# Optimization experiments

Hardware: AMD Instinct MI355X
Metric: run time of the kernel (lower is better)

Reference implementation:

```python
import jax, jax.numpy as jnp
import numpy as np

B, N, M, C1, C2 = 8, 8192, 2048, 64, 128
MLP = [128, 128]
EPS = 1e-5


def setup_inputs() -> dict:
    key = jax.random.key(0)
    ks = jax.random.split(key, 12)
    inp = {
        'low_theta': jax.random.normal(ks[0], (B, N), jnp.float32),
        'low_phi': jax.random.normal(ks[1], (B, N), jnp.float32),
        'low_feats': jax.random.normal(ks[2], (B, C1, N), jnp.float32),
        'high_theta': jax.random.normal(ks[3], (B, M), jnp.float32),
        'high_phi': jax.random.normal(ks[4], (B, M), jnp.float32),
        'high_feats': jax.random.normal(ks[5], (B, C2, M), jnp.float32),
    }
    in_ch = C1 + C2
    # layer 0: conv1d (kernel size 1) -> weight [out, in], bias [out]; BN gamma/beta
    inp['W0'] = jax.random.normal(ks[6], (MLP[0], in_ch), jnp.float32) * 0.05
    inp['b0'] = jnp.zeros((MLP[0],), jnp.float32)
    inp['g0'] = jnp.ones((MLP[0],), jnp.float32)
    inp['beta0'] = jnp.zeros((MLP[0],), jnp.float32)
    # layer 1
    inp['W1'] = jax.random.normal(ks[7], (MLP[1], MLP[0]), jnp.float32) * 0.05
    inp['b1'] = jnp.zeros((MLP[1],), jnp.float32)
    inp['g1'] = jnp.ones((MLP[1],), jnp.float32)
    inp['beta1'] = jnp.zeros((MLP[1],), jnp.float32)
    return inp


def _conv_bn_relu(x, W, b, gamma, beta):
    # x: [B, Cin, N] -> 1x1 conv -> BN (training-mode batch stats, biased var) -> ReLU
    y = jnp.einsum('oi,bin->bon', W, x) + b[None, :, None]
    mean = jnp.mean(y, axis=(0, 2), keepdims=True)
    var = jnp.mean((y - mean) ** 2, axis=(0, 2), keepdims=True)
    yhat = (y - mean) * jax.lax.rsqrt(var + EPS)
    return jax.nn.relu(gamma[None, :, None] * yhat + beta[None, :, None])


def reference(low_theta, low_phi, low_feats, high_theta, high_phi, high_feats,
              W0, b0, g0, beta0, W1, b1, g1, beta1):
    # pairwise angular distance [B, N, M]
    dtheta = low_theta[:, :, None] - high_theta[:, None, :]
    dphi = low_phi[:, :, None] - high_phi[:, None, :]
    dist = jnp.sqrt(dtheta ** 2 + dphi ** 2)
    idx = jnp.argmin(dist, axis=-1)  # [B, N]
    # gather nearest-neighbor high features -> [B, C2, N]
    c2 = high_feats.shape[1]
    interpolated = jnp.take_along_axis(
        high_feats, jnp.broadcast_to(idx[:, None, :], (idx.shape[0], c2, idx.shape[1])), axis=2)
    cat = jnp.concatenate([low_feats, interpolated], axis=1)  # [B, C1+C2, N]
    h = _conv_bn_relu(cat, W0, b0, g0, beta0)
    out = _conv_bn_relu(h, W1, b1, g1, beta1)
    return out
```

## Files before the change

### kernel.cpp

```cpp
#include <hip/hip_runtime.h>
#include <hip/hip_bf16.h>

#define BB 8
#define NN 8192
#define MM 2048
#define C1 64
#define C2 128
#define CIN 192
#define CO 128
#define NB (BB*NN)
#define EPS 1e-5f

typedef unsigned short u16;
typedef unsigned int u32;
typedef __bf16 bf16_t;
typedef bf16_t bf16x8 __attribute__((ext_vector_type(8)));
typedef float f32x4 __attribute__((ext_vector_type(4)));

static __device__ __forceinline__ float b2f(u16 u) { return __uint_as_float(((u32)u) << 16); }
static __device__ __forceinline__ u16 f2b(float f) {
    __hip_bfloat16 h = __float2bfloat16(f);
    u16 u; __builtin_memcpy(&u, &h, 2); return u;
}

__global__ void k_prep_w(const float* __restrict__ W0, const float* __restrict__ W1,
                         u16* __restrict__ W0b, u16* __restrict__ W1b) {
    int t = blockIdx.x * 256 + threadIdx.x;
    if (t < CIN * CO) W0b[t] = f2b(W0[t]);
    if (t < CO * CO)  W1b[t] = f2b(W1[t]);
}

__global__ void k_prep_h(const float* __restrict__ hf, u16* __restrict__ hT) {
    __shared__ u16 s[64][65];
    int b = blockIdx.x, m0 = blockIdx.y * 64, c0 = blockIdx.z * 64;
    for (int e = threadIdx.x; e < 64 * 64; e += 256) {
        int i = e >> 6, j = e & 63;
        s[i][j] = f2b(hf[(b * C2 + c0 + i) * MM + m0 + j]);
    }
    __syncthreads();
    for (int e = threadIdx.x; e < 64 * 64; e += 256) {
        int ii = e & 63, jj = e >> 6;
        hT[(b * MM + m0 + jj) * C2 + c0 + ii] = s[ii][jj];
    }
}

__global__ __launch_bounds__(256) void k_argmin(
        const float* __restrict__ lt_, const float* __restrict__ lp_,
        const float* __restrict__ ht_, const float* __restrict__ hp_,
        int* __restrict__ idx) {
    __shared__ float2 hs[8 * 260];
    int b = blockIdx.x >> 8;
    int n0 = (blockIdx.x & 255) << 5;
    int tid = threadIdx.x;
    for (int e = tid; e < MM; e += 256) {
        int p = e >> 8, i = e & 255;
        hs[p * 260 + i] = make_float2(ht_[b * MM + e], hp_[b * MM + e]);
    }
    __syncthreads();
    int q = tid >> 3, p = tid & 7;
    float lt = lt_[b * NN + n0 + q];
    float lp = lp_[b * NN + n0 + q];
    float dl[4] = {1e30f, 1e30f, 1e30f, 1e30f};
    float dpv[4] = {1e30f, 1e30f, 1e30f, 1e30f};
    int il[4] = {0, 0, 0, 0}, ip[4] = {0, 0, 0, 0};
    const float2* hp2 = &hs[p * 260];
    int mbase = p << 8;
#pragma unroll 8
    for (int i4 = 0; i4 < 64; ++i4) {
#pragma unroll
        for (int c = 0; c < 4; ++c) {
            float2 h = hp2[i4 * 4 + c];
            float dt = lt - h.x, dp = lp - h.y;
            float d2 = __fadd_rn(__fmul_rn(dt, dt), __fmul_rn(dp, dp));
            bool hit = d2 < dl[c];
            dpv[c] = hit ? dl[c] : dpv[c];
            ip[c] = hit ? il[c] : ip[c];
            dl[c] = hit ? d2 : dl[c];
            il[c] = hit ? mbase + i4 * 4 + c : il[c];
        }
    }
    float bs = 1e30f; int bm = 0x7fffffff;
#pragma unroll
    for (int c = 0; c < 4; ++c) {
        float sl = __fsqrt_rn(dl[c]);
        float sp = __fsqrt_rn(dpv[c]);
        int cand = (sp == sl) ? ip[c] : il[c];
        if (sl < bs || (sl == bs && cand < bm)) { bs = sl; bm = cand; }
    }
#pragma unroll
    for (int d = 1; d <= 4; d <<= 1) {
        float ov = __shfl_xor(bs, d, 64);
        int om = __shfl_xor(bm, d, 64);
        if (ov < bs || (ov == bs && om < bm)) { bs = ov; bm = om; }
    }
    if (p == 0) idx[b * NN + n0 + q] = bm;
}

static __device__ __forceinline__ void epilogue(
        f32x4* ac0, f32x4* ac1, const float* bias, u16* yl,
        float* chs, float* chq, int w, int ln, int q) {
#pragma unroll
    for (int mf = 0; mf < 2; ++mf) {
        f32x4* A = mf ? ac1 : ac0;
        int chb = 32 * w + 16 * mf + 4 * q;
        float bs[4], ss[4] = {0.f, 0.f, 0.f, 0.f}, sq[4] = {0.f, 0.f, 0.f, 0.f};
#pragma unroll
        for (int r = 0; r < 4; ++r) bs[r] = bias[chb + r];
#pragma unroll
        for (int nf = 0; nf < 4; ++nf) {
            int n = (nf << 4) + ln;
#pragma unroll
            for (int r = 0; r < 4; ++r) {
                float y = A[nf][r] + bs[r];
                ss[r] += y; sq[r] += y * y;
                int o = chb + r;
                yl[(o << 6) + (n ^ ((o & 7) << 3))] = f2b(y);
            }
        }
#pragma unroll
        for (int r = 0; r < 4; ++r) {
            float v = ss[r], u2 = sq[r];
#pragma unroll
            for (int d = 1; d < 16; d <<= 1) {
                v += __shfl_xor(v, d, 64);
                u2 += __shfl_xor(u2, d, 64);
            }
            if (ln == 0) { atomicAdd(&chs[chb + r], v); atomicAdd(&chq[chb + r], u2); }
        }
    }
}

__global__ __launch_bounds__(256) void k_red(const float* __restrict__ gpart,
                                             float* __restrict__ gout) {
    __shared__ float part[4];
    int c = blockIdx.x;
    int t = threadIdx.x;
    float s = 0.f;
#pragma unroll
    for (int k = 0; k < 4; ++k)
        s += gpart[(t + (k << 8)) * 256 + c];
#pragma unroll
    for (int d = 1; d < 64; d <<= 1)
        s += __shfl_xor(s, d, 64);
    if ((t & 63) == 0) part[t >> 6] = s;
    __syncthreads();
    if (t == 0) gout[c] = (part[0] + part[1]) + (part[2] + part[3]);
}

__global__ __launch_bounds__(256) void k_l0(
        const float* __restrict__ lf, const u16* __restrict__ hT, const int* __restrict__ idx,
        const u16* __restrict__ W0b, const float* __restrict__ b0,
        u16* __restrict__ y0, float* __restrict__ gpart) {
    __shared__ u16 xt[64 * CIN];
    __shared__ u16 ylds[CO * 64];
    __shared__ float chs[CO], chq[CO];
    __shared__ int idxs[64];
    int tid = threadIdx.x;
    int l = tid & 63, w = tid >> 6, ln = l & 15, q = l >> 4;
    int b = blockIdx.x >> 7, n0 = (blockIdx.x & 127) << 6;
    if (tid < 64) idxs[tid] = idx[b * NN + n0 + tid];
    if (tid < 128) { chs[tid] = 0.f; chq[tid] = 0.f; }
    __syncthreads();
    {
        const float* src = lf + (size_t)(b * C1 + l) * NN + n0 + (w << 4);
        float4 f0 = *(const float4*)src;
        float4 f1 = *(const float4*)(src + 4);
        float4 f2 = *(const float4*)(src + 8);
        float4 f3 = *(const float4*)(src + 12);
        float v[16] = {f0.x, f0.y, f0.z, f0.w, f1.x, f1.y, f1.z, f1.w,
                       f2.x, f2.y, f2.z, f2.w, f3.x, f3.y, f3.z, f3.w};
        int cc = l >> 3, clo = l & 7;
#pragma unroll
        for (int i = 0; i < 16; ++i) {
            int n = (w << 4) + i;
            xt[n * CIN + ((cc ^ (i & 7)) << 3) + clo] = f2b(v[i]);
        }
    }
    for (int e = tid; e < 1024; e += 256) {
        int n = e >> 4, c16 = e & 15;
        uint4 v = *(const uint4*)(hT + (size_t)(b * MM + idxs[n]) * C2 + (c16 << 3));
        *(uint4*)&xt[n * CIN + (((8 + c16) ^ (n & 7)) << 3)] = v;
    }
    __syncthreads();
    f32x4 ac0[4], ac1[4];
#pragma unroll
    for (int nf = 0; nf < 4; ++nf) {
        ac0[nf] = f32x4{0.f, 0.f, 0.f, 0.f};
        ac1[nf] = f32x4{0.f, 0.f, 0.f, 0.f};
    }
    const u16* w0r0 = W0b + (32 * w + ln) * CIN + 8 * q;
    const u16* w0r1 = w0r0 + 16 * CIN;
#pragma unroll
    for (int s = 0; s < 6; ++s) {
        bf16x8 a0 = *(const bf16x8*)(w0r0 + 32 * s);
        bf16x8 a1 = *(const bf16x8*)(w0r1 + 32 * s);
#pragma unroll
        for (int nf = 0; nf < 4; ++nf) {
            bf16x8 bv = *(const bf16x8*)&xt[(16 * nf + ln) * CIN + (((4 * s + q) ^ (ln & 7)) << 3)];
            ac0[nf] = __builtin_amdgcn_mfma_f32_16x16x32_bf16(a0, bv, ac0[nf], 0, 0, 0);
            ac1[nf] = __builtin_amdgcn_mfma_f32_16x16x32_bf16(a1, bv, ac1[nf], 0, 0, 0);
        }
    }
    epilogue(ac0, ac1, b0, ylds, chs, chq, w, ln, q);
    __syncthreads();
    gpart[blockIdx.x * 256 + tid] = (tid < 128) ? chs[tid] : chq[tid - 128];
    {
        int o = tid >> 1, h = tid & 1;
#pragma unroll
        for (int jj = 0; jj < 4; ++jj) {
            int j = (h << 2) + jj;
            uint4 v = *(const uint4*)&ylds[(o << 6) + ((j ^ (o & 7)) << 3)];
            *(uint4*)(y0 + (size_t)(b * CO + o) * NN + n0 + (j << 3)) = v;
        }
    }
}

__global__ __launch_bounds__(256) void k_l1(
        u16* __restrict__ y, const float* __restrict__ g0, const float* __restrict__ be0,
        const u16* __restrict__ W1b, const float* __restrict__ b1,
        const float* __restrict__ gstat, float* __restrict__ gpart) {
    __shared__ u16 xt[64 * CO];
    __shared__ u16 ylds[CO * 64];
    __shared__ float chs[CO], chq[CO], sc[CO], sh[CO];
    int tid = threadIdx.x;
    int l = tid & 63, w = tid >> 6, ln = l & 15, q = l >> 4;
    int b = blockIdx.x >> 7, n0 = (blockIdx.x & 127) << 6;
    if (tid < 128) {
        float s = gstat[tid], qv = gstat[128 + tid];
        float mu = s * (1.f / NB);
        float var = qv * (1.f / NB) - mu * mu;
        float istd = 1.f / __fsqrt_rn(var + EPS);
        float scale = g0[tid] * istd;
        sc[tid] = scale;
        sh[tid] = be0[tid] - mu * scale;
        chs[tid] = 0.f; chq[tid] = 0.f;
    }
    __syncthreads();
#pragma unroll
    for (int it = 0; it < 2; ++it) {
        int c = (it << 6) + l;
        const u16* src = y + (size_t)(b * CO + c) * NN + n0 + (w << 4);
        uint4 r0 = *(const uint4*)src;
        uint4 r1 = *(const uint4*)(src + 8);
        u16 raw[16];
        *(uint4*)&raw[0] = r0;
        *(uint4*)&raw[8] = r1;
        float scale = sc[c], shift = sh[c];
        int cc = c >> 3, clo = c & 7;
#pragma unroll
        for (int i = 0; i < 16; ++i) {
            int n = (w << 4) + i;
            float hv = fmaxf(b2f(raw[i]) * scale + shift, 0.f);
            xt[(n << 7) + ((cc ^ (i & 7)) << 3) + clo] = f2b(hv);
        }
    }
    __syncthreads();
    f32x4 ac0[4], ac1[4];
#pragma unroll
    for (int nf = 0; nf < 4; ++nf) {
        ac0[nf] = f32x4{0.f, 0.f, 0.f, 0.f};
        ac1[nf] = f32x4{0.f, 0.f, 0.f, 0.f};
    }
    const u16* w1r0 = W1b + (32 * w + ln) * CO + 8 * q;
    const u16* w1r1 = w1r0 + 16 * CO;
#pragma unroll
    for (int s = 0; s < 4; ++s) {
        bf16x8 a0 = *(const bf16x8*)(w1r0 + 32 * s);
        bf16x8 a1 = *(const bf16x8*)(w1r1 + 32 * s);
#pragma unroll
        for (int nf = 0; nf < 4; ++nf) {
            bf16x8 bv = *(const bf16x8*)&xt[((16 * nf + ln) << 7) + (((4 * s + q) ^ (ln & 7)) << 3)];
            ac0[nf] = __builtin_amdgcn_mfma_f32_16x16x32_bf16(a0, bv, ac0[nf], 0, 0, 0);
            ac1[nf] = __builtin_amdgcn_mfma_f32_16x16x32_bf16(a1, bv, ac1[nf], 0, 0, 0);
        }
    }
    epilogue(ac0, ac1, b1, ylds, chs, chq, w, ln, q);
    __syncthreads();
    gpart[blockIdx.x * 256 + tid] = (tid < 128) ? chs[tid] : chq[tid - 128];
    {
        int o = tid >> 1, h = tid & 1;
#pragma unroll
        for (int jj = 0; jj < 4; ++jj) {
            int j = (h << 2) + jj;
            uint4 v = *(const uint4*)&ylds[(o << 6) + ((j ^ (o & 7)) << 3)];
            *(uint4*)(y + (size_t)(b * CO + o) * NN + n0 + (j << 3)) = v;
        }
    }
}

__global__ __launch_bounds__(256) void k_bn1(
        const u16* __restrict__ y, const float* __restrict__ gstat,
        const float* __restrict__ g1, const float* __restrict__ be1,
        float* __restrict__ out) {
    int t = blockIdx.x * 256 + threadIdx.x;
    int o = (t >> 10) & 127;
    float s = gstat[256 + o], qv = gstat[384 + o];
    float mu = s * (1.f / NB);
    float var = qv * (1.f / NB) - mu * mu;
    float istd = 1.f / __fsqrt_rn(var + EPS);
    float scale = g1[o] * istd;
    float shift = be1[o] - mu * scale;
    size_t e0 = (size_t)t << 3;
    uint4 v = *(const uint4*)(y + e0);
    u16 raw[8];
    *(uint4*)raw = v;
    float r[8];
#pragma unroll
    for (int k = 0; k < 8; ++k)
        r[k] = fmaxf(b2f(raw[k]) * scale + shift, 0.f);
    *(float4*)(out + e0) = make_float4(r[0], r[1], r[2], r[3]);
    *(float4*)(out + e0 + 4) = make_float4(r[4], r[5], r[6], r[7]);
}

extern "C" void kernel_launch(void* const* d_in, const int* in_sizes, int n_in,
                              void* d_out, int out_size, void* d_ws, size_t ws_size,
                              hipStream_t stream) {
    const float* lt = (const float*)d_in[0];
    const float* lp = (const float*)d_in[1];
    const float* lf = (const float*)d_in[2];
    const float* ht = (const float*)d_in[3];
    const float* hp = (const float*)d_in[4];
    const float* hf = (const float*)d_in[5];
    const float* W0 = (const float*)d_in[6];
    const float* b0 = (const float*)d_in[7];
    const float* g0 = (const float*)d_in[8];
    const float* be0 = (const float*)d_in[9];
    const float* W1 = (const float*)d_in[10];
    const float* b1 = (const float*)d_in[11];
    const float* g1 = (const float*)d_in[12];
    const float* be1 = (const float*)d_in[13];

    char* ws = (char*)d_ws;
    u16* y0 = (u16*)ws;
    u16* hT = (u16*)(ws + 16777216);
    int* idx = (int*)(ws + 20971520);
    float* gstat = (float*)(ws + 21233664);
    u16* W0b = (u16*)(ws + 21235712);
    u16* W1b = (u16*)(ws + 21284864);
    float* gpart = (float*)(ws + 21317632);

    k_prep_w<<<96, 256, 0, stream>>>(W0, W1, W0b, W1b);
    k_prep_h<<<dim3(8, 32, 2), 256, 0, stream>>>(hf, hT);
    k_argmin<<<2048, 256, 0, stream>>>(lt, lp, ht, hp, idx);
    k_l0<<<1024, 256, 0, stream>>>(lf, hT, idx, W0b, b0, y0, gpart);
    k_red<<<256, 256, 0, stream>>>(gpart, gstat);
    k_l1<<<1024, 256, 0, stream>>>(y0, g0, be0, W1b, b1, gstat, gpart);
    k_red<<<256, 256, 0, stream>>>(gpart, gstat + 256);
    k_bn1<<<4096, 256, 0, stream>>>(y0, gstat, g1, be1, (float*)d_out);
}
```

Before: 110.2 us.

## Register-block four queries per thread in argmin and use packed FP32 math

The nearest-neighbour argmin kernel now has each thread handle four low-resolution points against its slice of high points instead of one. This reuses each LDS load of high coordinates across four queries and lets the block count drop by four. The difference-and-square step uses packed v_pk_add/v_pk_mul FP32 instructions on coordinate pairs. In exchange it needs more registers per thread, gives fewer blocks for latency hiding, and the ordering and tie handling inside each slice change.

```diff
diff --git a/kernel.cpp b/kernel.cpp
--- a/kernel.cpp
+++ b/kernel.cpp
@@ -16,6 +16,7 @@
 typedef __bf16 bf16_t;
 typedef bf16_t bf16x8 __attribute__((ext_vector_type(8)));
 typedef float f32x4 __attribute__((ext_vector_type(4)));
+typedef float f32x2 __attribute__((ext_vector_type(2)));
 
 static __device__ __forceinline__ float b2f(u16 u) { return __uint_as_float(((u32)u) << 16); }
 static __device__ __forceinline__ u16 f2b(float f) {
@@ -49,51 +50,69 @@
         const float* __restrict__ ht_, const float* __restrict__ hp_,
         int* __restrict__ idx) {
     __shared__ float2 hs[8 * 260];
-    int b = blockIdx.x >> 8;
-    int n0 = (blockIdx.x & 255) << 5;
+    int b = blockIdx.x >> 6;
+    int n0 = (blockIdx.x & 63) << 7;
     int tid = threadIdx.x;
     for (int e = tid; e < MM; e += 256) {
         int p = e >> 8, i = e & 255;
         hs[p * 260 + i] = make_float2(ht_[b * MM + e], hp_[b * MM + e]);
     }
     __syncthreads();
-    int q = tid >> 3, p = tid & 7;
-    float lt = lt_[b * NN + n0 + q];
-    float lp = lp_[b * NN + n0 + q];
-    float dl[4] = {1e30f, 1e30f, 1e30f, 1e30f};
+    int g = tid >> 3, p = tid & 7;
+    int qbase = n0 + (g << 2);
+    f32x2 nq[4];
+#pragma unroll
+    for (int j = 0; j < 4; ++j) {
+        nq[j][0] = -lt_[b * NN + qbase + j];
+        nq[j][1] = -lp_[b * NN + qbase + j];
+    }
+    float dl[4]  = {1e30f, 1e30f, 1e30f, 1e30f};
     float dpv[4] = {1e30f, 1e30f, 1e30f, 1e30f};
-    int il[4] = {0, 0, 0, 0}, ip[4] = {0, 0, 0, 0};
+    int il[4] = {0, 0, 0, 0}, ipx[4] = {0, 0, 0, 0};
     const float2* hp2 = &hs[p * 260];
+#pragma unroll 4
+    for (int k = 0; k < 128; ++k) {
+        f32x4 v = *(const f32x4*)&hp2[k * 2];
+        f32x2 c0, c1;
+        c0[0] = v[0]; c0[1] = v[1];
+        c1[0] = v[2]; c1[1] = v[3];
+        int i0 = k * 2;
+#pragma unroll
+        for (int j = 0; j < 4; ++j) {
+            f32x2 e0, e1;
+            asm("v_pk_add_f32 %0, %1, %2" : "=v"(e0) : "v"(c0), "v"(nq[j]));
+            asm("v_pk_mul_f32 %0, %1, %2" : "=v"(e0) : "v"(e0), "v"(e0));
+            float d2a = __fadd_rn(e0[0], e0[1]);
+            bool h0 = d2a < dl[j];
+            dpv[j] = h0 ? dl[j] : dpv[j];
+            ipx[j] = h0 ? il[j] : ipx[j];
+            dl[j]  = h0 ? d2a : dl[j];
+            il[j]  = h0 ? i0 : il[j];
+            asm("v_pk_add_f32 %0, %1, %2" : "=v"(e1) : "v"(c1), "v"(nq[j]));
+            asm("v_pk_mul_f32 %0, %1, %2" : "=v"(e1) : "v"(e1), "v"(e1));
+            float d2b = __fadd_rn(e1[0], e1[1]);
+            bool h1 = d2b < dl[j];
+            dpv[j] = h1 ? dl[j] : dpv[j];
+            ipx[j] = h1 ? il[j] : ipx[j];
+            dl[j]  = h1 ? d2b : dl[j];
+            il[j]  = h1 ? i0 + 1 : il[j];
+        }
+    }
     int mbase = p << 8;
-#pragma unroll 8
-    for (int i4 = 0; i4 < 64; ++i4) {
-#pragma unroll
-        for (int c = 0; c < 4; ++c) {
-            float2 h = hp2[i4 * 4 + c];
-            float dt = lt - h.x, dp = lp - h.y;
-            float d2 = __fadd_rn(__fmul_rn(dt, dt), __fmul_rn(dp, dp));
-            bool hit = d2 < dl[c];
-            dpv[c] = hit ? dl[c] : dpv[c];
-            ip[c] = hit ? il[c] : ip[c];
-            dl[c] = hit ? d2 : dl[c];
-            il[c] = hit ? mbase + i4 * 4 + c : il[c];
-        }
-    }
-    float bs = 1e30f; int bm = 0x7fffffff;
-#pragma unroll
-    for (int c = 0; c < 4; ++c) {
-        float sl = __fsqrt_rn(dl[c]);
-        float sp = __fsqrt_rn(dpv[c]);
-        int cand = (sp == sl) ? ip[c] : il[c];
-        if (sl < bs || (sl == bs && cand < bm)) { bs = sl; bm = cand; }
-    }
-#pragma unroll
-    for (int d = 1; d <= 4; d <<= 1) {
-        float ov = __shfl_xor(bs, d, 64);
-        int om = __shfl_xor(bm, d, 64);
-        if (ov < bs || (ov == bs && om < bm)) { bs = ov; bm = om; }
-    }
-    if (p == 0) idx[b * NN + n0 + q] = bm;
+#pragma unroll
+    for (int j = 0; j < 4; ++j) {
+        float sl = __fsqrt_rn(dl[j]);
+        float sp = __fsqrt_rn(dpv[j]);
+        int bm = mbase + ((sp == sl) ? ipx[j] : il[j]);
+        float bs = sl;
+#pragma unroll
+        for (int d = 1; d <= 4; d <<= 1) {
+            float ov = __shfl_xor(bs, d, 64);
+            int om = __shfl_xor(bm, d, 64);
+            if (ov < bs || (ov == bs && om < bm)) { bs = ov; bm = om; }
+        }
+        if (p == 0) idx[b * NN + qbase + j] = bm;
+    }
 }
 
 static __device__ __forceinline__ void epilogue(
@@ -341,7 +360,7 @@
 
     k_prep_w<<<96, 256, 0, stream>>>(W0, W1, W0b, W1b);
     k_prep_h<<<dim3(8, 32, 2), 256, 0, stream>>>(hf, hT);
-    k_argmin<<<2048, 256, 0, stream>>>(lt, lp, ht, hp, idx);
+    k_argmin<<<512, 256, 0, stream>>>(lt, lp, ht, hp, idx);
     k_l0<<<1024, 256, 0, stream>>>(lf, hT, idx, W0b, b0, y0, gpart);
     k_red<<<256, 256, 0, stream>>>(gpart, gstat);
     k_l1<<<1024, 256, 0, stream>>>(y0, g0, be0, W1b, b1, gstat, gpart);
```

After: 115.5 us. 4.8% more time.
